# Performance work log

Measured on AMD Instinct MI355X. Metric: run time of the kernel, lower is better.

The kernel has to match this reference:

```python
import jax, jax.numpy as jnp
import numpy as np

T, H, I, E, SI, TOP_K = 1024, 2048, 1408, 60, 5632, 4


def setup_inputs() -> dict:
    key = jax.random.key(0)
    ks = jax.random.split(key, 9)
    s = 0.02  # typical init scale for weights
    return {
        "x": jax.random.normal(ks[0], (T, H), jnp.float32),
        "router_w": jax.random.normal(ks[1], (E, H), jnp.float32) * s,
        "w_gate": jax.random.normal(ks[2], (E, I, H), jnp.float32) * s,
        "w_up": jax.random.normal(ks[3], (E, I, H), jnp.float32) * s,
        "w_down": jax.random.normal(ks[4], (E, H, I), jnp.float32) * s,
        "sw_gate": jax.random.normal(ks[5], (SI, H), jnp.float32) * s,
        "sw_up": jax.random.normal(ks[6], (SI, H), jnp.float32) * s,
        "sw_down": jax.random.normal(ks[7], (H, SI), jnp.float32) * s,
        "shared_gate_w": jax.random.normal(ks[8], (1, H), jnp.float32) * s,
        "top_k": TOP_K,
    }


def reference(x, router_w, w_gate, w_up, w_down, sw_gate, sw_up, sw_down, shared_gate_w, top_k):
    Ttok, Hdim = x.shape
    Eexp = router_w.shape[0]
    # --- router: softmax over experts, top-k selection (norm_topk_prob=False) ---
    logits = x @ router_w.T                          # [T,E]
    probs = jax.nn.softmax(logits, axis=-1)
    topk_p, topk_i = jax.lax.top_k(probs, top_k)     # [T,k]
    # dense combine weights: zero for unrouted experts
    combine = jnp.zeros((Ttok, Eexp), x.dtype)
    combine = combine.at[jnp.arange(Ttok)[:, None], topk_i].set(topk_p)  # [T,E]

    # --- routed experts: SwiGLU MLP per expert, weighted accumulate (scan over E) ---
    def expert_step(acc, w):
        wg, wu, wd, c = w                            # [I,H],[I,H],[H,I],[T]
        h = jax.nn.silu(x @ wg.T) * (x @ wu.T)       # [T,I]
        return acc + c[:, None] * (h @ wd.T), None

    moe_out, _ = jax.lax.scan(expert_step, jnp.zeros_like(x),
                              (w_gate, w_up, w_down, combine.T))

    # --- shared expert with sigmoid gate ---
    shared = (jax.nn.silu(x @ sw_gate.T) * (x @ sw_up.T)) @ sw_down.T    # [T,H]
    shared = jax.nn.sigmoid(x @ shared_gate_w.T) * shared                # [T,1]*[T,H]
    return moe_out + shared
```

## Files before the change

kernel.cpp:

```cpp
#include <hip/hip_runtime.h>
#include <hip/hip_bf16.h>


typedef float  f32x4  __attribute__((ext_vector_type(4)));
typedef short  bf16x8 __attribute__((ext_vector_type(8)));
typedef unsigned short u16;
typedef unsigned int   u32;

constexpr int TT = 1024, HD = 2048, ID = 1408, NE = 60, SID = 5632, KTOP = 4;

#define GLDS(g, l) __builtin_amdgcn_global_load_lds( \
    (const __attribute__((address_space(1))) void*)(g), \
    (__attribute__((address_space(3))) void*)(l), 16, 0, 0)
#define WAITVM(n) asm volatile("s_waitcnt vmcnt(" #n ")" ::: "memory")
#define BAR() do { asm volatile("" ::: "memory"); \
    __builtin_amdgcn_s_barrier(); \
    asm volatile("" ::: "memory"); } while (0)

__device__ __forceinline__ u16 f2bf(float f) {
    union { float f; u32 u; } v; v.f = f;
    u32 r = v.u + 0x7FFFu + ((v.u >> 16) & 1u);
    return (u16)(r >> 16);
}
__device__ __forceinline__ u32 cvtpk(float a, float b) {
    u32 r; asm("v_cvt_pk_bf16_f32 %0, %1, %2" : "=v"(r) : "v"(a), "v"(b));
    return r;
}
__device__ __forceinline__ bf16x8 cvt8(float4 a, float4 b) {
    union { u32 u[4]; bf16x8 v; } rr;
    rr.u[0] = cvtpk(a.x, a.y); rr.u[1] = cvtpk(a.z, a.w);
    rr.u[2] = cvtpk(b.x, b.y); rr.u[3] = cvtpk(b.z, b.w);
    return rr.v;
}

__global__ void zero_k(int* __restrict__ p) { p[threadIdx.x] = 0; }

__global__ __launch_bounds__(256) void xcvt_k(const float* __restrict__ x, u16* __restrict__ xb)
{
    size_t i = ((size_t)blockIdx.x * 256 + threadIdx.x) * 16;
    const float4* p = (const float4*)(x + i);
    float4 f0 = p[0], f1 = p[1], f2 = p[2], f3 = p[3];
    uint4 o0, o1;
    o0.x = cvtpk(f0.x, f0.y); o0.y = cvtpk(f0.z, f0.w);
    o0.z = cvtpk(f1.x, f1.y); o0.w = cvtpk(f1.z, f1.w);
    o1.x = cvtpk(f2.x, f2.y); o1.y = cvtpk(f2.z, f2.w);
    o1.z = cvtpk(f3.x, f3.y); o1.w = cvtpk(f3.z, f3.w);
    ((uint4*)(xb + i))[0] = o0;
    ((uint4*)(xb + i))[1] = o1;
}

__global__ __launch_bounds__(64) void router_k(
    const float* __restrict__ x, const float* __restrict__ rw,
    const float* __restrict__ sgw,
    float* __restrict__ topk_p, int* __restrict__ topk_i,
    int* __restrict__ cnt, float* __restrict__ sgate)
{
    const int t = blockIdx.x, l = threadIdx.x;
    const float4* xr = ((const float4*)(x + (size_t)t * HD)) + l * 8;
    float4 xa[8];
    #pragma unroll
    for (int i = 0; i < 8; i++) xa[i] = xr[i];

    float le = 0.f;
    for (int e = 0; e < NE; e++) {
        const float4* wr = ((const float4*)(rw + (size_t)e * HD)) + l * 8;
        float a = 0.f;
        #pragma unroll
        for (int i = 0; i < 8; i++) {
            float4 wv = wr[i];
            a += xa[i].x * wv.x + xa[i].y * wv.y + xa[i].z * wv.z + xa[i].w * wv.w;
        }
        #pragma unroll
        for (int s = 32; s; s >>= 1) a += __shfl_xor(a, s);
        if (l == e) le = a;
    }
    {
        const float4* wr = ((const float4*)sgw) + l * 8;
        float a = 0.f;
        #pragma unroll
        for (int i = 0; i < 8; i++) {
            float4 wv = wr[i];
            a += xa[i].x * wv.x + xa[i].y * wv.y + xa[i].z * wv.z + xa[i].w * wv.w;
        }
        #pragma unroll
        for (int s = 32; s; s >>= 1) a += __shfl_xor(a, s);
        if (l == 0) sgate[t] = 1.f / (1.f + __expf(-a));
    }
    float mv = (l < NE) ? le : -3.4e38f;
    #pragma unroll
    for (int s = 32; s; s >>= 1) mv = fmaxf(mv, __shfl_xor(mv, s));
    float p = (l < NE) ? __expf(le - mv) : 0.f;
    float ss = p;
    #pragma unroll
    for (int s = 32; s; s >>= 1) ss += __shfl_xor(ss, s);
    p /= ss;
    float pv = (l < NE) ? p : -1.f;
    int   pi = l;
    float kp = 0.f; int ki = 0;
    for (int k = 0; k < KTOP; k++) {
        float bv = pv; int bi = pi;
        #pragma unroll
        for (int s = 32; s; s >>= 1) {
            float ov = __shfl_xor(bv, s); int oi = __shfl_xor(bi, s);
            if (ov > bv || (ov == bv && oi < bi)) { bv = ov; bi = oi; }
        }
        if (l == k) { kp = bv; ki = bi; }
        if (pi == bi) pv = -1.f;
    }
    if (l < KTOP) {
        topk_p[t * KTOP + l] = kp;
        topk_i[t * KTOP + l] = ki;
        atomicAdd(&cnt[ki], 1);
    }
}

__global__ __launch_bounds__(64) void prefix_k(const int* __restrict__ cnt, int* __restrict__ base)
{
    int l = threadIdx.x;
    if (l < NE) {
        int s = 0;
        for (int j = 0; j < l; j++) s += cnt[j];
        base[l] = s;
    }
}

__global__ __launch_bounds__(256) void scatter_k(
    const float* __restrict__ topk_p, const int* __restrict__ topk_i,
    const int* __restrict__ base, int* __restrict__ fill,
    int* __restrict__ slot_tok, float* __restrict__ slot_wt)
{
    int t = blockIdx.x * blockDim.x + threadIdx.x;
    if (t >= TT) return;
    for (int k = 0; k < KTOP; k++) {
        int e = topk_i[t * KTOP + k];
        int pos = atomicAdd(&fill[e], 1);
        int s = base[e] + pos;
        slot_tok[s] = t;
        slot_wt[s]  = topk_p[t * KTOP + k];
    }
}

template<bool GROUPED>
__global__ __launch_bounds__(256, 3) void gu_k(
    const u16* __restrict__ Xb,
    const float* __restrict__ Wg, const float* __restrict__ Wu, size_t bStride,
    u16* __restrict__ H,
    const int* __restrict__ slot_tok, const float* __restrict__ slot_wt,
    const int* __restrict__ cnt, const int* __restrict__ basearr,
    int K, int N)
{
    __shared__ u16   Asl[2][128 * 32];
    __shared__ float Bgsl[2][64 * 32];
    __shared__ float Busl[2][64 * 32];

    const int tid = threadIdx.x, w = tid >> 6, lane = tid & 63;
    const int lm = lane & 15, lk = lane >> 4;
    const int wm0 = (w >> 1) * 64, wn0 = (w & 1) * 32;
    const int e = GROUPED ? blockIdx.z : 0;
    const int mcnt = GROUPED ? cnt[e] : 128;
    const int mbase = GROUPED ? basearr[e] : 0;

    const int aCh = ((lane & 3) ^ ((lane >> 2) & 3)) << 3;
    const int bCh = ((lane & 7) ^ ((lane >> 3) & 7)) << 2;

    const float* bgSrc[2]; const float* buSrc[2];
    #pragma unroll
    for (int j = 0; j < 2; j++) {
        size_t rB = (size_t)(blockIdx.x * 64 + w * 16 + j * 8 + (lane >> 3));
        bgSrc[j] = Wg + (size_t)e * bStride + rB * K + bCh;
        buSrc[j] = Wu + (size_t)e * bStride + rB * K + bCh;
    }

    int aOff[4], bOff[2][2];
    #pragma unroll
    for (int mf = 0; mf < 4; mf++) {
        int r = wm0 + mf * 16 + lm;
        aOff[mf] = r * 32 + ((lk ^ (r & 3)) << 3);
    }
    #pragma unroll
    for (int nf = 0; nf < 2; nf++) {
        int rb = wn0 + nf * 16 + lm;
        bOff[nf][0] = rb * 32 + ((((lk << 1)    ) ^ (rb & 7)) << 2);
        bOff[nf][1] = rb * 32 + ((((lk << 1) | 1) ^ (rb & 7)) << 2);
    }

    const int nk = K >> 5;

    for (int mt = 0; GROUPED ? (mt * 128 < mcnt) : (mt == 0); ++mt) {
        const u16* aSrc[2];
        #pragma unroll
        for (int j = 0; j < 2; j++) {
            int mrow = w * 32 + j * 16 + (lane >> 2);
            int row;
            if constexpr (GROUPED) {
                int sl = mbase + mt * 128 + mrow;
                row = (mt * 128 + mrow < mcnt) ? slot_tok[sl] : slot_tok[mbase];
            } else row = blockIdx.y * 128 + mrow;
            aSrc[j] = Xb + (size_t)row * K + aCh;
        }

        f32x4 acc[2][4][2];
        #pragma unroll
        for (int m = 0; m < 2; m++)
            #pragma unroll
            for (int mf = 0; mf < 4; mf++)
                #pragma unroll
                for (int nf = 0; nf < 2; nf++)
                    acc[m][mf][nf] = f32x4{0.f, 0.f, 0.f, 0.f};

        auto stage = [&](int b, int kt) {
            #pragma unroll
            for (int j = 0; j < 2; j++)
                GLDS(aSrc[j] + kt, &Asl[b][(w * 32 + j * 16) * 32]);
            #pragma unroll
            for (int j = 0; j < 2; j++) {
                GLDS(bgSrc[j] + kt, &Bgsl[b][(w * 16 + j * 8) * 32]);
                GLDS(buSrc[j] + kt, &Busl[b][(w * 16 + j * 8) * 32]);
            }
        };

        stage(0, 0);
        for (int t = 0; t < nk; ++t) {
            const int cur = t & 1;
            if (t + 1 < nk) { stage(cur ^ 1, (t + 1) << 5); WAITVM(6); }
            else WAITVM(0);
            BAR();
            const u16*   At  = Asl[cur];
            const float* Bgt = Bgsl[cur];
            const float* But = Busl[cur];
            bf16x8 af[4];
            #pragma unroll
            for (int mf = 0; mf < 4; mf++) af[mf] = *(const bf16x8*)&At[aOff[mf]];
            #pragma unroll
            for (int nf = 0; nf < 2; nf++) {
                bf16x8 bg = cvt8(*(const float4*)&Bgt[bOff[nf][0]],
                                 *(const float4*)&Bgt[bOff[nf][1]]);
                bf16x8 bu = cvt8(*(const float4*)&But[bOff[nf][0]],
                                 *(const float4*)&But[bOff[nf][1]]);
                #pragma unroll
                for (int mf = 0; mf < 4; mf++) {
                    acc[0][mf][nf] = __builtin_amdgcn_mfma_f32_16x16x32_bf16(af[mf], bg, acc[0][mf][nf], 0, 0, 0);
                    acc[1][mf][nf] = __builtin_amdgcn_mfma_f32_16x16x32_bf16(af[mf], bu, acc[1][mf][nf], 0, 0, 0);
                }
            }
            BAR();
        }

        #pragma unroll
        for (int mf = 0; mf < 4; mf++)
            #pragma unroll
            for (int j = 0; j < 4; j++) {
                int m = wm0 + mf * 16 + lk * 4 + j;
                bool valid = GROUPED ? (mt * 128 + m < mcnt) : true;
                if (valid) {
                    size_t row; float wt;
                    if constexpr (GROUPED) {
                        size_t sl = (size_t)(mbase + mt * 128 + m);
                        row = sl; wt = slot_wt[sl];
                    } else { row = (size_t)(blockIdx.y * 128 + m); wt = 1.f; }
                    #pragma unroll
                    for (int nf = 0; nf < 2; nf++) {
                        int col = blockIdx.x * 64 + wn0 + nf * 16 + lm;
                        float g = acc[0][mf][nf][j], u = acc[1][mf][nf][j];
                        float hv = g / (1.f + __expf(-g)) * u * wt;
                        H[row * (size_t)N + col] = f2bf(hv);
                    }
                }
            }
    }
}

template<bool GROUPED>
__global__ __launch_bounds__(256, 4) void down_k(
    const u16* __restrict__ Hb, const float* __restrict__ W0, size_t bStride,
    float* __restrict__ outF,
    const int* __restrict__ slot_tok, const float* __restrict__ sgate,
    const int* __restrict__ cnt, const int* __restrict__ basearr,
    int K, int N)
{
    __shared__ u16   Asl[2][128 * 32];
    __shared__ float Bsl[2][64 * 32];

    const int tid = threadIdx.x, w = tid >> 6, lane = tid & 63;
    const int lm = lane & 15, lk = lane >> 4;
    const int wm0 = (w >> 1) * 64, wn0 = (w & 1) * 32;
    const int e = GROUPED ? blockIdx.z : 0;
    const int mcnt = GROUPED ? cnt[e] : 128;
    const int mbase = GROUPED ? basearr[e] : 0;

    const int aCh = ((lane & 3) ^ ((lane >> 2) & 3)) << 3;
    const int bCh = ((lane & 7) ^ ((lane >> 3) & 7)) << 2;

    const float* bSrc[2];
    #pragma unroll
    for (int j = 0; j < 2; j++) {
        size_t rB = (size_t)(blockIdx.x * 64 + w * 16 + j * 8 + (lane >> 3));
        bSrc[j] = W0 + (size_t)e * bStride + rB * K + bCh;
    }

    int aOff[4], bOff[2][2];
    #pragma unroll
    for (int mf = 0; mf < 4; mf++) {
        int r = wm0 + mf * 16 + lm;
        aOff[mf] = r * 32 + ((lk ^ (r & 3)) << 3);
    }
    #pragma unroll
    for (int nf = 0; nf < 2; nf++) {
        int rb = wn0 + nf * 16 + lm;
        bOff[nf][0] = rb * 32 + ((((lk << 1)    ) ^ (rb & 7)) << 2);
        bOff[nf][1] = rb * 32 + ((((lk << 1) | 1) ^ (rb & 7)) << 2);
    }

    const int nk = K >> 5;

    for (int mt = 0; GROUPED ? (mt * 128 < mcnt) : (mt == 0); ++mt) {
        const u16* aSrc[2];
        #pragma unroll
        for (int j = 0; j < 2; j++) {
            int mrow = w * 32 + j * 16 + (lane >> 2);
            size_t row;
            if constexpr (GROUPED) row = (size_t)(mbase + mt * 128 + mrow);
            else                   row = (size_t)(blockIdx.y * 128 + mrow);
            aSrc[j] = Hb + row * K + aCh;
        }

        f32x4 acc[4][2];
        #pragma unroll
        for (int mf = 0; mf < 4; mf++)
            #pragma unroll
            for (int nf = 0; nf < 2; nf++)
                acc[mf][nf] = f32x4{0.f, 0.f, 0.f, 0.f};

        auto stage = [&](int b, int kt) {
            #pragma unroll
            for (int j = 0; j < 2; j++)
                GLDS(aSrc[j] + kt, &Asl[b][(w * 32 + j * 16) * 32]);
            #pragma unroll
            for (int j = 0; j < 2; j++)
                GLDS(bSrc[j] + kt, &Bsl[b][(w * 16 + j * 8) * 32]);
        };

        stage(0, 0);
        for (int t = 0; t < nk; ++t) {
            const int cur = t & 1;
            if (t + 1 < nk) { stage(cur ^ 1, (t + 1) << 5); WAITVM(4); }
            else WAITVM(0);
            BAR();
            const u16*   At = Asl[cur];
            const float* Bt = Bsl[cur];
            bf16x8 af[4];
            #pragma unroll
            for (int mf = 0; mf < 4; mf++) af[mf] = *(const bf16x8*)&At[aOff[mf]];
            #pragma unroll
            for (int nf = 0; nf < 2; nf++) {
                bf16x8 bf_ = cvt8(*(const float4*)&Bt[bOff[nf][0]],
                                  *(const float4*)&Bt[bOff[nf][1]]);
                #pragma unroll
                for (int mf = 0; mf < 4; mf++)
                    acc[mf][nf] = __builtin_amdgcn_mfma_f32_16x16x32_bf16(af[mf], bf_, acc[mf][nf], 0, 0, 0);
            }
            BAR();
        }

        #pragma unroll
        for (int mf = 0; mf < 4; mf++)
            #pragma unroll
            for (int j = 0; j < 4; j++) {
                int m = wm0 + mf * 16 + lk * 4 + j;
                bool valid = GROUPED ? (mt * 128 + m < mcnt) : true;
                if (valid) {
                    #pragma unroll
                    for (int nf = 0; nf < 2; nf++) {
                        int col = blockIdx.x * 64 + wn0 + nf * 16 + lm;
                        if constexpr (GROUPED) {
                            int tok = slot_tok[mbase + mt * 128 + m];
                            atomicAdd(&outF[(size_t)tok * N + col], acc[mf][nf][j]);
                        } else {
                            int tok = blockIdx.y * 128 + m;
                            outF[(size_t)tok * N + col] = sgate[tok] * acc[mf][nf][j];
                        }
                    }
                }
            }
    }
}

extern "C" void kernel_launch(void* const* d_in, const int* in_sizes, int n_in,
                              void* d_out, int out_size, void* d_ws, size_t ws_size,
                              hipStream_t stream)
{
    const float* x      = (const float*)d_in[0];
    const float* rw     = (const float*)d_in[1];
    const float* w_gate = (const float*)d_in[2];
    const float* w_up   = (const float*)d_in[3];
    const float* w_down = (const float*)d_in[4];
    const float* sw_g   = (const float*)d_in[5];
    const float* sw_u   = (const float*)d_in[6];
    const float* sw_d   = (const float*)d_in[7];
    const float* sgw    = (const float*)d_in[8];
    float* out = (float*)d_out;

    char* ws = (char*)d_ws;
    int*   cnt      = (int*)(ws + 0);
    int*   fill     = (int*)(ws + 256);
    int*   basea    = (int*)(ws + 512);
    float* sgate    = (float*)(ws + 768);
    float* topk_p   = (float*)(ws + 5120);
    int*   topk_i   = (int*)(ws + 21504);
    int*   slot_tok = (int*)(ws + 37888);
    float* slot_wt  = (float*)(ws + 54272);
    u16*   xb = (u16*)(ws + 71680);
    u16*   h  = xb + (size_t)TT * HD;
    u16*   hs = h + (size_t)(4096 + 128) * ID;

    zero_k<<<1, 128, 0, stream>>>(cnt);
    xcvt_k<<<512, 256, 0, stream>>>(x, xb);
    router_k<<<TT, 64, 0, stream>>>(x, rw, sgw, topk_p, topk_i, cnt, sgate);
    prefix_k<<<1, 64, 0, stream>>>(cnt, basea);
    scatter_k<<<4, 256, 0, stream>>>(topk_p, topk_i, basea, fill, slot_tok, slot_wt);

    gu_k<true><<<dim3(ID / 64, 1, NE), 256, 0, stream>>>(
        xb, w_gate, w_up, (size_t)ID * HD, h,
        slot_tok, slot_wt, cnt, basea, HD, ID);
    gu_k<false><<<dim3(SID / 64, TT / 128, 1), 256, 0, stream>>>(
        xb, sw_g, sw_u, 0, hs,
        nullptr, nullptr, nullptr, nullptr, HD, SID);
    down_k<false><<<dim3(HD / 64, TT / 128, 1), 256, 0, stream>>>(
        hs, sw_d, 0, out,
        nullptr, sgate, nullptr, nullptr, SID, HD);
    down_k<true><<<dim3(HD / 64, 1, NE), 256, 0, stream>>>(
        h, w_down, (size_t)HD * ID, out,
        slot_tok, nullptr, cnt, basea, ID, HD);
}
```

Measured before the change: 802.5 us.

## Merge routed and shared expert GEMMs into single launches with triple-buffered down pass

Fuses the routed-expert and shared-expert gate/up GEMMs into one launch and the two down-projection GEMMs into another, using a flat block index to pick the role. This removes the tail gaps between back-to-back launches and lets the irregular per-expert blocks overlap with the dense shared-expert blocks. The down kernel also moves from double to triple buffering, and the A-tile LDS swizzle gains an extra XOR term to reduce bank conflicts. The shared down path now uses atomicAdd into an output that must be zeroed by a new kernel first, which adds an extra pass over the output and atomic traffic.

```diff
diff --git a/kernel.cpp b/kernel.cpp
--- a/kernel.cpp
+++ b/kernel.cpp
@@ -8,6 +8,10 @@
 typedef unsigned int   u32;
 
 constexpr int TT = 1024, HD = 2048, ID = 1408, NE = 60, SID = 5632, KTOP = 4;
+constexpr int NBR_GU = (ID / 64) * NE;
+constexpr int NB_GU  = NBR_GU + (SID / 64) * (TT / 128);
+constexpr int NBS_DN = (HD / 64) * (TT / 128);
+constexpr int NB_DN  = NBS_DN + (HD / 64) * NE;
 
 #define GLDS(g, l) __builtin_amdgcn_global_load_lds( \
     (const __attribute__((address_space(1))) void*)(g), \
@@ -34,6 +38,10 @@
 }
 
 __global__ void zero_k(int* __restrict__ p) { p[threadIdx.x] = 0; }
+
+__global__ __launch_bounds__(256) void zeroout_k(float* __restrict__ p) {
+    ((float4*)p)[blockIdx.x * 256 + threadIdx.x] = make_float4(0.f, 0.f, 0.f, 0.f);
+}
 
 __global__ __launch_bounds__(256) void xcvt_k(const float* __restrict__ x, u16* __restrict__ xb)
 {
@@ -140,42 +148,53 @@
     }
 }
 
-template<bool GROUPED>
-__global__ __launch_bounds__(256, 3) void gu_k(
+__global__ __launch_bounds__(256, 3) void gu_all(
     const u16* __restrict__ Xb,
-    const float* __restrict__ Wg, const float* __restrict__ Wu, size_t bStride,
-    u16* __restrict__ H,
+    const float* __restrict__ w_gate, const float* __restrict__ w_up,
+    const float* __restrict__ sw_g, const float* __restrict__ sw_u,
+    u16* __restrict__ h, u16* __restrict__ hs,
     const int* __restrict__ slot_tok, const float* __restrict__ slot_wt,
-    const int* __restrict__ cnt, const int* __restrict__ basearr,
-    int K, int N)
+    const int* __restrict__ cnt, const int* __restrict__ basea)
 {
     __shared__ u16   Asl[2][128 * 32];
     __shared__ float Bgsl[2][64 * 32];
     __shared__ float Busl[2][64 * 32];
 
+    const int bid = blockIdx.x;
+    const bool grouped = bid < NBR_GU;
     const int tid = threadIdx.x, w = tid >> 6, lane = tid & 63;
     const int lm = lane & 15, lk = lane >> 4;
     const int wm0 = (w >> 1) * 64, wn0 = (w & 1) * 32;
-    const int e = GROUPED ? blockIdx.z : 0;
-    const int mcnt = GROUPED ? cnt[e] : 128;
-    const int mbase = GROUPED ? basearr[e] : 0;
-
-    const int aCh = ((lane & 3) ^ ((lane >> 2) & 3)) << 3;
+
+    int e = 0, my = 0, nb;
+    const float *Wg, *Wu; u16* Hout; int Nout;
+    if (grouped) {
+        e = bid / 22; nb = bid % 22;
+        Wg = w_gate + (size_t)e * ID * HD; Wu = w_up + (size_t)e * ID * HD;
+        Hout = h; Nout = ID;
+    } else {
+        int sid = bid - NBR_GU; my = sid / 88; nb = sid % 88;
+        Wg = sw_g; Wu = sw_u; Hout = hs; Nout = SID;
+    }
+    const int mcnt  = grouped ? cnt[e] : 128;
+    const int mbase = grouped ? basea[e] : 0;
+
+    const int aCh = (((lane & 3) ^ ((lane >> 2) & 3) ^ ((lane >> 4) & 3))) << 3;
     const int bCh = ((lane & 7) ^ ((lane >> 3) & 7)) << 2;
 
     const float* bgSrc[2]; const float* buSrc[2];
     #pragma unroll
     for (int j = 0; j < 2; j++) {
-        size_t rB = (size_t)(blockIdx.x * 64 + w * 16 + j * 8 + (lane >> 3));
-        bgSrc[j] = Wg + (size_t)e * bStride + rB * K + bCh;
-        buSrc[j] = Wu + (size_t)e * bStride + rB * K + bCh;
+        size_t rB = (size_t)(nb * 64 + w * 16 + j * 8 + (lane >> 3));
+        bgSrc[j] = Wg + rB * HD + bCh;
+        buSrc[j] = Wu + rB * HD + bCh;
     }
 
     int aOff[4], bOff[2][2];
     #pragma unroll
     for (int mf = 0; mf < 4; mf++) {
         int r = wm0 + mf * 16 + lm;
-        aOff[mf] = r * 32 + ((lk ^ (r & 3)) << 3);
+        aOff[mf] = r * 32 + ((lk ^ (r & 3) ^ ((r >> 2) & 3)) << 3);
     }
     #pragma unroll
     for (int nf = 0; nf < 2; nf++) {
@@ -184,29 +203,29 @@
         bOff[nf][1] = rb * 32 + ((((lk << 1) | 1) ^ (rb & 7)) << 2);
     }
 
-    const int nk = K >> 5;
-
-    for (int mt = 0; GROUPED ? (mt * 128 < mcnt) : (mt == 0); ++mt) {
+    const int nk = HD >> 5;
+
+    for (int mt = 0; grouped ? (mt * 128 < mcnt) : (mt == 0); ++mt) {
         const u16* aSrc[2];
         #pragma unroll
         for (int j = 0; j < 2; j++) {
             int mrow = w * 32 + j * 16 + (lane >> 2);
             int row;
-            if constexpr (GROUPED) {
+            if (grouped) {
                 int sl = mbase + mt * 128 + mrow;
                 row = (mt * 128 + mrow < mcnt) ? slot_tok[sl] : slot_tok[mbase];
-            } else row = blockIdx.y * 128 + mrow;
-            aSrc[j] = Xb + (size_t)row * K + aCh;
-        }
-
-        f32x4 acc[2][4][2];
-        #pragma unroll
-        for (int m = 0; m < 2; m++)
-            #pragma unroll
-            for (int mf = 0; mf < 4; mf++)
-                #pragma unroll
-                for (int nf = 0; nf < 2; nf++)
-                    acc[m][mf][nf] = f32x4{0.f, 0.f, 0.f, 0.f};
+            } else row = my * 128 + mrow;
+            aSrc[j] = Xb + (size_t)row * HD + aCh;
+        }
+
+        f32x4 accG[4][2], accU[4][2];
+        #pragma unroll
+        for (int mf = 0; mf < 4; mf++)
+            #pragma unroll
+            for (int nf = 0; nf < 2; nf++) {
+                accG[mf][nf] = f32x4{0.f, 0.f, 0.f, 0.f};
+                accU[mf][nf] = f32x4{0.f, 0.f, 0.f, 0.f};
+            }
 
         auto stage = [&](int b, int kt) {
             #pragma unroll
@@ -239,8 +258,8 @@
                                  *(const float4*)&But[bOff[nf][1]]);
                 #pragma unroll
                 for (int mf = 0; mf < 4; mf++) {
-                    acc[0][mf][nf] = __builtin_amdgcn_mfma_f32_16x16x32_bf16(af[mf], bg, acc[0][mf][nf], 0, 0, 0);
-                    acc[1][mf][nf] = __builtin_amdgcn_mfma_f32_16x16x32_bf16(af[mf], bu, acc[1][mf][nf], 0, 0, 0);
+                    accG[mf][nf] = __builtin_amdgcn_mfma_f32_16x16x32_bf16(af[mf], bg, accG[mf][nf], 0, 0, 0);
+                    accU[mf][nf] = __builtin_amdgcn_mfma_f32_16x16x32_bf16(af[mf], bu, accU[mf][nf], 0, 0, 0);
                 }
             }
             BAR();
@@ -251,58 +270,67 @@
             #pragma unroll
             for (int j = 0; j < 4; j++) {
                 int m = wm0 + mf * 16 + lk * 4 + j;
-                bool valid = GROUPED ? (mt * 128 + m < mcnt) : true;
+                bool valid = grouped ? (mt * 128 + m < mcnt) : true;
                 if (valid) {
                     size_t row; float wt;
-                    if constexpr (GROUPED) {
+                    if (grouped) {
                         size_t sl = (size_t)(mbase + mt * 128 + m);
                         row = sl; wt = slot_wt[sl];
-                    } else { row = (size_t)(blockIdx.y * 128 + m); wt = 1.f; }
+                    } else { row = (size_t)(my * 128 + m); wt = 1.f; }
                     #pragma unroll
                     for (int nf = 0; nf < 2; nf++) {
-                        int col = blockIdx.x * 64 + wn0 + nf * 16 + lm;
-                        float g = acc[0][mf][nf][j], u = acc[1][mf][nf][j];
+                        int col = nb * 64 + wn0 + nf * 16 + lm;
+                        float g = accG[mf][nf][j], u = accU[mf][nf][j];
                         float hv = g / (1.f + __expf(-g)) * u * wt;
-                        H[row * (size_t)N + col] = f2bf(hv);
+                        Hout[row * (size_t)Nout + col] = f2bf(hv);
                     }
                 }
             }
     }
 }
 
-template<bool GROUPED>
-__global__ __launch_bounds__(256, 4) void down_k(
-    const u16* __restrict__ Hb, const float* __restrict__ W0, size_t bStride,
+__global__ __launch_bounds__(256, 3) void down_all(
+    const u16* __restrict__ h, const u16* __restrict__ hs,
+    const float* __restrict__ w_down, const float* __restrict__ sw_d,
     float* __restrict__ outF,
     const int* __restrict__ slot_tok, const float* __restrict__ sgate,
-    const int* __restrict__ cnt, const int* __restrict__ basearr,
-    int K, int N)
-{
-    __shared__ u16   Asl[2][128 * 32];
-    __shared__ float Bsl[2][64 * 32];
-
+    const int* __restrict__ cnt, const int* __restrict__ basea)
+{
+    __shared__ u16   Asl[3][128 * 32];
+    __shared__ float Bsl[3][64 * 32];
+
+    const int bid = blockIdx.x;
+    const bool shared_m = bid < NBS_DN;
     const int tid = threadIdx.x, w = tid >> 6, lane = tid & 63;
     const int lm = lane & 15, lk = lane >> 4;
     const int wm0 = (w >> 1) * 64, wn0 = (w & 1) * 32;
-    const int e = GROUPED ? blockIdx.z : 0;
-    const int mcnt = GROUPED ? cnt[e] : 128;
-    const int mbase = GROUPED ? basearr[e] : 0;
-
-    const int aCh = ((lane & 3) ^ ((lane >> 2) & 3)) << 3;
+
+    int e = 0, my = 0, nb, K;
+    const u16* Ap; const float* Wp;
+    if (shared_m) {
+        my = bid / 32; nb = bid % 32; K = SID; Ap = hs; Wp = sw_d;
+    } else {
+        int rid = bid - NBS_DN; e = rid / 32; nb = rid % 32; K = ID;
+        Ap = h; Wp = w_down + (size_t)e * HD * ID;
+    }
+    const int mcnt  = shared_m ? 128 : cnt[e];
+    const int mbase = shared_m ? 0 : basea[e];
+
+    const int aCh = (((lane & 3) ^ ((lane >> 2) & 3) ^ ((lane >> 4) & 3))) << 3;
     const int bCh = ((lane & 7) ^ ((lane >> 3) & 7)) << 2;
 
     const float* bSrc[2];
     #pragma unroll
     for (int j = 0; j < 2; j++) {
-        size_t rB = (size_t)(blockIdx.x * 64 + w * 16 + j * 8 + (lane >> 3));
-        bSrc[j] = W0 + (size_t)e * bStride + rB * K + bCh;
+        size_t rB = (size_t)(nb * 64 + w * 16 + j * 8 + (lane >> 3));
+        bSrc[j] = Wp + rB * K + bCh;
     }
 
     int aOff[4], bOff[2][2];
     #pragma unroll
     for (int mf = 0; mf < 4; mf++) {
         int r = wm0 + mf * 16 + lm;
-        aOff[mf] = r * 32 + ((lk ^ (r & 3)) << 3);
+        aOff[mf] = r * 32 + ((lk ^ (r & 3) ^ ((r >> 2) & 3)) << 3);
     }
     #pragma unroll
     for (int nf = 0; nf < 2; nf++) {
@@ -313,23 +341,21 @@
 
     const int nk = K >> 5;
 
-    for (int mt = 0; GROUPED ? (mt * 128 < mcnt) : (mt == 0); ++mt) {
+    for (int mt = 0; shared_m ? (mt == 0) : (mt * 128 < mcnt); ++mt) {
         const u16* aSrc[2];
         #pragma unroll
         for (int j = 0; j < 2; j++) {
             int mrow = w * 32 + j * 16 + (lane >> 2);
-            size_t row;
-            if constexpr (GROUPED) row = (size_t)(mbase + mt * 128 + mrow);
-            else                   row = (size_t)(blockIdx.y * 128 + mrow);
-            aSrc[j] = Hb + row * K + aCh;
+            size_t row = shared_m ? (size_t)(my * 128 + mrow)
+                                  : (size_t)(mbase + mt * 128 + mrow);
+            aSrc[j] = Ap + row * K + aCh;
         }
 
         f32x4 acc[4][2];
         #pragma unroll
         for (int mf = 0; mf < 4; mf++)
             #pragma unroll
-            for (int nf = 0; nf < 2; nf++)
-                acc[mf][nf] = f32x4{0.f, 0.f, 0.f, 0.f};
+            for (int nf = 0; nf < 2; nf++) acc[mf][nf] = f32x4{0.f, 0.f, 0.f, 0.f};
 
         auto stage = [&](int b, int kt) {
             #pragma unroll
@@ -339,15 +365,9 @@
             for (int j = 0; j < 2; j++)
                 GLDS(bSrc[j] + kt, &Bsl[b][(w * 16 + j * 8) * 32]);
         };
-
-        stage(0, 0);
-        for (int t = 0; t < nk; ++t) {
-            const int cur = t & 1;
-            if (t + 1 < nk) { stage(cur ^ 1, (t + 1) << 5); WAITVM(4); }
-            else WAITVM(0);
-            BAR();
-            const u16*   At = Asl[cur];
-            const float* Bt = Bsl[cur];
+        auto comp = [&](int b) {
+            const u16*   At = Asl[b];
+            const float* Bt = Bsl[b];
             bf16x8 af[4];
             #pragma unroll
             for (int mf = 0; mf < 4; mf++) af[mf] = *(const bf16x8*)&At[aOff[mf]];
@@ -359,26 +379,33 @@
                 for (int mf = 0; mf < 4; mf++)
                     acc[mf][nf] = __builtin_amdgcn_mfma_f32_16x16x32_bf16(af[mf], bf_, acc[mf][nf], 0, 0, 0);
             }
-            BAR();
-        }
+        };
+
+        stage(0, 0); stage(1, 32);
+        int t = 0, cb = 0;
+        for (; t + 2 < nk; ++t) {
+            int sbuf = cb - 1; if (sbuf < 0) sbuf += 3;
+            stage(sbuf, (t + 2) << 5);
+            WAITVM(8); BAR(); comp(cb); BAR();
+            cb = (cb + 1 == 3) ? 0 : cb + 1;
+        }
+        WAITVM(4); BAR(); comp(cb); BAR();
+        cb = (cb + 1 == 3) ? 0 : cb + 1;
+        WAITVM(0); BAR(); comp(cb); BAR();
 
         #pragma unroll
         for (int mf = 0; mf < 4; mf++)
             #pragma unroll
             for (int j = 0; j < 4; j++) {
                 int m = wm0 + mf * 16 + lk * 4 + j;
-                bool valid = GROUPED ? (mt * 128 + m < mcnt) : true;
-                if (valid) {
+                if (mt * 128 + m < mcnt) {
+                    int tok; float scale;
+                    if (shared_m) { tok = my * 128 + m; scale = sgate[tok]; }
+                    else          { tok = slot_tok[mbase + mt * 128 + m]; scale = 1.f; }
                     #pragma unroll
                     for (int nf = 0; nf < 2; nf++) {
-                        int col = blockIdx.x * 64 + wn0 + nf * 16 + lm;
-                        if constexpr (GROUPED) {
-                            int tok = slot_tok[mbase + mt * 128 + m];
-                            atomicAdd(&outF[(size_t)tok * N + col], acc[mf][nf][j]);
-                        } else {
-                            int tok = blockIdx.y * 128 + m;
-                            outF[(size_t)tok * N + col] = sgate[tok] * acc[mf][nf][j];
-                        }
+                        int col = nb * 64 + wn0 + nf * 16 + lm;
+                        atomicAdd(&outF[(size_t)tok * HD + col], scale * acc[mf][nf][j]);
                     }
                 }
             }
@@ -414,21 +441,17 @@
     u16*   hs = h + (size_t)(4096 + 128) * ID;
 
     zero_k<<<1, 128, 0, stream>>>(cnt);
+    zeroout_k<<<TT * HD / 1024, 256, 0, stream>>>(out);
     xcvt_k<<<512, 256, 0, stream>>>(x, xb);
     router_k<<<TT, 64, 0, stream>>>(x, rw, sgw, topk_p, topk_i, cnt, sgate);
     prefix_k<<<1, 64, 0, stream>>>(cnt, basea);
     scatter_k<<<4, 256, 0, stream>>>(topk_p, topk_i, basea, fill, slot_tok, slot_wt);
 
-    gu_k<true><<<dim3(ID / 64, 1, NE), 256, 0, stream>>>(
-        xb, w_gate, w_up, (size_t)ID * HD, h,
-        slot_tok, slot_wt, cnt, basea, HD, ID);
-    gu_k<false><<<dim3(SID / 64, TT / 128, 1), 256, 0, stream>>>(
-        xb, sw_g, sw_u, 0, hs,
-        nullptr, nullptr, nullptr, nullptr, HD, SID);
-    down_k<false><<<dim3(HD / 64, TT / 128, 1), 256, 0, stream>>>(
-        hs, sw_d, 0, out,
-        nullptr, sgate, nullptr, nullptr, SID, HD);
-    down_k<true><<<dim3(HD / 64, 1, NE), 256, 0, stream>>>(
-        h, w_down, (size_t)HD * ID, out,
-        slot_tok, nullptr, cnt, basea, ID, HD);
-}
+    gu_all<<<NB_GU, 256, 0, stream>>>(
+        xb, w_gate, w_up, sw_g, sw_u, h, hs,
+        slot_tok, slot_wt, cnt, basea);
+
+    down_all<<<NB_DN, 256, 0, stream>>>(
+        h, hs, w_down, sw_d, out,
+        slot_tok, sgate, cnt, basea);
+}
```

After: 727.8 us. -9.3%, faster.
